# Kernel tuning notes

Hardware: AMD Instinct MI355X
Metric: run time of the kernel (lower is better)

## Reference

```python
import jax, jax.numpy as jnp
import numpy as np


def setup_inputs() -> dict:
    key = jax.random.key(0)
    L, N, Q, C = 6, 64, 64, 256
    hs_pair = jax.random.normal(key, (L, N, Q, C), dtype=jnp.float32)
    return {"hs_pair": hs_pair}


def _merge_step(centers):
    # centers: [L, N, Q, C] -> [L, N, Q-1, C]
    L, N, Q, C = centers.shape
    # pairwise Euclidean distance via gram matrix (avoids [L,N,Q,Q,C] diff tensor)
    sq = jnp.sum(centers * centers, axis=-1)                      # [L,N,Q]
    gram = jnp.einsum('lnqc,lnpc->lnqp', centers, centers)        # [L,N,Q,Q]
    d2 = sq[..., :, None] + sq[..., None, :] - 2.0 * gram
    dist = jnp.sqrt(jnp.maximum(d2, 0.0))                         # [L,N,Q,Q]
    dist = dist + jnp.max(dist) * jnp.eye(Q, dtype=dist.dtype)
    idx = jnp.argmin(dist.reshape(L, N, Q * Q), axis=2)           # [L,N]
    x, y = idx // Q, idx % Q                                      # row-major argmin => x < y
    cx = jnp.take_along_axis(centers, x[:, :, None, None], axis=2)[:, :, 0]  # [L,N,C]
    cy = jnp.take_along_axis(centers, y[:, :, None, None], axis=2)[:, :, 0]  # [L,N,C]
    merged = (cx + cy) * 0.5
    last = centers[:, :, -1]                                      # [L,N,C]
    qr = jnp.arange(Q)
    mask_x = (qr[None, None, :] == x[:, :, None])[..., None]      # [L,N,Q,1]
    mask_y = (qr[None, None, :] == y[:, :, None])[..., None]
    centers = jnp.where(mask_x, merged[:, :, None, :], centers)
    centers = jnp.where(mask_y, last[:, :, None, :], centers)
    return centers[:, :, :-1]


def reference(hs_pair):
    centers = hs_pair
    Q0 = centers.shape[2]
    # Q-2 sequential merges; each iteration has a distinct static shape,
    # so a Python loop (unrolled under jit) is the correct structure.
    for _ in range(Q0 - 2):
        centers = _merge_step(centers)
    return centers  # [L, N, 2, C]
```

## Files before the change

### kernel.cpp

```cpp
#include <hip/hip_runtime.h>
#include <stdint.h>

#define NSLICE 384
#define QMAX   64
#define CDIM   256
#define NTHR   512

#define SW(r,c) ((r)*QMAX + ((c)^(r)))

__device__ __forceinline__ float dpp_sum64(float v) {
#define DPP_ADD(c) v += __int_as_float(__builtin_amdgcn_update_dpp(0, __float_as_int(v), c, 0xf, 0xf, true))
    DPP_ADD(0x111);
    DPP_ADD(0x112);
    DPP_ADD(0x114);
    DPP_ADD(0x118);
    DPP_ADD(0x142);
    DPP_ADD(0x143);
#undef DPP_ADD
    return v;
}

template<int CTRL>
__device__ __forceinline__ unsigned dpp_min_step(unsigned v) {
    unsigned o = (unsigned)__builtin_amdgcn_update_dpp((int)v, (int)v, CTRL, 0xf, 0xf, false);
    return v < o ? v : o;
}

__device__ __forceinline__ unsigned wave_min_bcast(unsigned v) {
    v = dpp_min_step<0x111>(v);
    v = dpp_min_step<0x112>(v);
    v = dpp_min_step<0x114>(v);
    v = dpp_min_step<0x118>(v);
    v = dpp_min_step<0x142>(v);
    v = dpp_min_step<0x143>(v);
    return (unsigned)__builtin_amdgcn_readlane((int)v, 63);
}

__device__ __forceinline__ unsigned oct_min_all(unsigned v) {
    v = dpp_min_step<0xB1>(v);
    v = dpp_min_step<0x4E>(v);
    v = dpp_min_step<0x124>(v);
    return v;
}

__launch_bounds__(NTHR, 4)
__global__ void hca_kernel(const float* __restrict__ in, float* __restrict__ out) {
    __shared__ __align__(16) float cen[QMAX * CDIM];
    __shared__ __align__(16) float dist[QMAX * QMAX];
    unsigned long long* const scratch = (unsigned long long*)(dist + 63 * QMAX);

    const int tid  = threadIdx.x;
    const int lane = tid & 63;
    const int w    = tid >> 6;
    const int slice = blockIdx.x;
    const float* src = in + (size_t)slice * (QMAX * CDIM);
    float* dst = out + (size_t)slice * (2 * CDIM);

    {
        const float4* s4 = (const float4*)src;
        float4* c4 = (float4*)cen;
        #pragma unroll
        for (int i = 0; i < (QMAX * CDIM / 4) / NTHR; ++i)
            c4[tid + i * NTHR] = s4[tid + i * NTHR];
    }
    __syncthreads();

    {
        float4 A[8];
        #pragma unroll
        for (int r = 0; r < 8; ++r)
            A[r] = ((const float4*)(cen + (w + 8 * r) * CDIM))[lane];

        #pragma unroll
        for (int r = 0; r < 8; ++r) {
            float t = A[r].x * A[r].x;
            t = fmaf(A[r].y, A[r].y, t); t = fmaf(A[r].z, A[r].z, t); t = fmaf(A[r].w, A[r].w, t);
            float s = dpp_sum64(t);
            if (lane == 63) dist[(w + 8 * r) * QMAX] = s;
        }
        __syncthreads();

        float sqq[8];
        #pragma unroll
        for (int r = 0; r < 8; ++r) sqq[r] = dist[(w + 8 * r) * QMAX];
        for (int p = 1; p < QMAX; ++p) {
            const float4 b = ((const float4*)(cen + p * CDIM))[lane];
            const float sqp = dist[p * QMAX];
            #pragma unroll
            for (int r = 0; r < 8; ++r) {
                const int q = w + 8 * r;
                if (q < p) {
                    float t = A[r].x * b.x;
                    t = fmaf(A[r].y, b.y, t); t = fmaf(A[r].z, b.z, t); t = fmaf(A[r].w, b.w, t);
                    float s = dpp_sum64(t);
                    if (lane == 63) {
                        float d2 = sqq[r] + sqp - 2.0f * s;
                        float d  = sqrtf(fmaxf(d2, 0.0f));
                        dist[SW(q, p)] = d;
                        dist[SW(p, q)] = d;
                    }
                }
            }
        }
    }
    __syncthreads();

    unsigned flat0, d0bits;
    {
        unsigned bdb = 0xFFFFFFFFu, bidx = 0xFFFu;
        for (int i = 0; i < 16; ++i) {
            float4 dv = ((const float4*)dist)[i * 64 + lane];
            const int rr  = 4 * i + (lane >> 4);
            const int cc0 = (lane & 15) * 4;
            #pragma unroll
            for (int e = 0; e < 4; ++e) {
                int cc = cc0 + e;
                int c  = cc ^ rr;
                unsigned db = __float_as_uint((&dv.x)[e]);
                unsigned idx = (unsigned)(rr * 64 + c);
                bool ok = (cc != 0);
                bool lt = ok & ((db < bdb) | ((db == bdb) & (idx < bidx)));
                bdb  = lt ? db : bdb;
                bidx = lt ? idx : bidx;
            }
        }
        d0bits = wave_min_bcast(bdb);
        unsigned cand = (bdb == d0bits) ? bidx : 0xFFFFFFFFu;
        flat0 = wave_min_bcast(cand);
    }
    __syncthreads();

    for (int Q = QMAX; Q > 2; --Q) {
        int x, y; unsigned dxyb;
        if (Q == QMAX) {
            x = (int)(flat0 >> 6); y = (int)(flat0 & 63); dxyb = d0bits;
        } else {
            unsigned long long k = scratch[lane & 7];
            unsigned hi = (unsigned)(k >> 32), lo = (unsigned)k;
            unsigned ghi = oct_min_all(hi);
            unsigned c2  = (hi == ghi) ? lo : 0xFFFFFFFFu;
            unsigned flat = oct_min_all(c2);
            x = (int)(flat >> 6); y = (int)(flat & 63);
            dxyb = ghi;
        }

        if (w == 0) {
            const int p = lane;
            const bool act = (p < Q - 1) && (p != x);
            const int p_old = (p == y) ? (Q - 1) : p;
            float dxp = 0.0f, dyp = 0.0f;
            if (act) {
                dxp = dist[SW(x, p_old)];
                dyp = dist[SW(y, p_old)];
            }
            const bool mv = (y != Q - 1) && (lane < Q - 1) && (lane != x) && (lane != y);
            float rowQ1 = 0.0f, colQ1 = 0.0f;
            if (mv) {
                rowQ1 = dist[SW(Q - 1, lane)];
                colQ1 = dist[SW(lane, Q - 1)];
            }
            const float dxy = __uint_as_float(dxyb);
            float t = 0.5f * (dxp * dxp + dyp * dyp) - 0.25f * (dxy * dxy);
            float d = sqrtf(fmaxf(t, 0.0f));
            if (mv) {
                dist[SW(y, lane)] = rowQ1;
                dist[SW(lane, y)] = colQ1;
            }
            if (act) {
                dist[SW(x, p)] = d;
                dist[SW(p, x)] = d;
            }
        }
        if (w == 1) {
            const float4 cx = ((const float4*)(cen + x * CDIM))[lane];
            const float4 cy = ((const float4*)(cen + y * CDIM))[lane];
            const float4 cq = ((const float4*)(cen + (Q - 1) * CDIM))[lane];
            float4 m;
            m.x = (cx.x + cy.x) * 0.5f; m.y = (cx.y + cy.y) * 0.5f;
            m.z = (cx.z + cy.z) * 0.5f; m.w = (cx.w + cy.w) * 0.5f;
            ((float4*)(cen + x * CDIM))[lane] = m;
            if (y != Q - 1)
                ((float4*)(cen + y * CDIM))[lane] = cq;
        }
        __syncthreads();

        if (Q > 3) {
            const int Qs = Q - 1;
            unsigned bdb = 0xFFFFFFFFu, bidx = 0xFFFu;
            #pragma unroll
            for (int ii = 0; ii < 2; ++ii) {
                const int i = 2 * w + ii;
                if (4 * i < Qs) {
                    float4 dv = ((const float4*)dist)[i * 64 + lane];
                    const int rr  = 4 * i + (lane >> 4);
                    const int cc0 = (lane & 15) * 4;
                    #pragma unroll
                    for (int e = 0; e < 4; ++e) {
                        int cc = cc0 + e;
                        int c  = cc ^ rr;
                        unsigned db = __float_as_uint((&dv.x)[e]);
                        unsigned idx = (unsigned)(rr * 64 + c);
                        bool ok = (rr < Qs) & (c < Qs) & (cc != 0);
                        bool lt = ok & ((db < bdb) | ((db == bdb) & (idx < bidx)));
                        bdb  = lt ? db : bdb;
                        bidx = lt ? idx : bidx;
                    }
                }
            }
            unsigned gd   = wave_min_bcast(bdb);
            unsigned cand = (bdb == gd) ? bidx : 0xFFFFFFFFu;
            unsigned gidx = wave_min_bcast(cand);
            if (lane == 0) scratch[w] = ((unsigned long long)gd << 32) | gidx;
        }
        __syncthreads();
    }

    for (int i = tid; i < 2 * CDIM; i += NTHR)
        dst[i] = cen[i];
}

extern "C" void kernel_launch(void* const* d_in, const int* in_sizes, int n_in,
                              void* d_out, int out_size, void* d_ws, size_t ws_size,
                              hipStream_t stream) {
    (void)in_sizes; (void)n_in; (void)d_ws; (void)ws_size; (void)out_size;
    const float* in = (const float*)d_in[0];
    float* out = (float*)d_out;
    hca_kernel<<<NSLICE, NTHR, 0, stream>>>(in, out);
}
```

Baseline: 136.0 us.

## Maintain per-row nearest-neighbor cache instead of full distance rescans each merge

Replaces the per-iteration full scan of the upper-triangular distance matrix with a per-row (min distance, column) cache held in double-buffered shared arrays placed in the freed last centroid row. Only rows whose cached nearest column was x or y, plus row x, are rescanned, spread across waves. The other rows are updated incrementally by comparing against the new distance to x. The global argmin then reduces the per-row keys with a wave-wide min. This cuts the O(Q^2) scan per step to roughly O(Q) work, at the cost of more complex bookkeeping and tie-ordering that must match the reference argmin exactly.

```diff
diff --git a/kernel.cpp b/kernel.cpp
--- a/kernel.cpp
+++ b/kernel.cpp
@@ -36,18 +36,14 @@
     return (unsigned)__builtin_amdgcn_readlane((int)v, 63);
 }
 
-__device__ __forceinline__ unsigned oct_min_all(unsigned v) {
-    v = dpp_min_step<0xB1>(v);
-    v = dpp_min_step<0x4E>(v);
-    v = dpp_min_step<0x124>(v);
-    return v;
-}
-
 __launch_bounds__(NTHR, 4)
 __global__ void hca_kernel(const float* __restrict__ in, float* __restrict__ out) {
     __shared__ __align__(16) float cen[QMAX * CDIM];
     __shared__ __align__(16) float dist[QMAX * QMAX];
-    unsigned long long* const scratch = (unsigned long long*)(dist + 63 * QMAX);
+    unsigned* const khi0 = (unsigned*)(cen + 63 * CDIM);
+    unsigned* const klo0 = khi0 + QMAX;
+    unsigned* const khi1 = khi0 + 2 * QMAX;
+    unsigned* const klo1 = khi0 + 3 * QMAX;
 
     const int tid  = threadIdx.x;
     const int lane = tid & 63;
@@ -135,13 +131,15 @@
         if (Q == QMAX) {
             x = (int)(flat0 >> 6); y = (int)(flat0 & 63); dxyb = d0bits;
         } else {
-            unsigned long long k = scratch[lane & 7];
-            unsigned hi = (unsigned)(k >> 32), lo = (unsigned)k;
-            unsigned ghi = oct_min_all(hi);
-            unsigned c2  = (hi == ghi) ? lo : 0xFFFFFFFFu;
-            unsigned flat = oct_min_all(c2);
-            x = (int)(flat >> 6); y = (int)(flat & 63);
-            dxyb = ghi;
+            const unsigned pr = (unsigned)((Q + 1) & 1);
+            const unsigned* khi_s = pr ? khi1 : khi0;
+            const unsigned* klo_s = pr ? klo1 : klo0;
+            unsigned hi = (lane < Q) ? khi_s[lane] : 0xFFFFFFFFu;
+            unsigned gd = wave_min_bcast(hi);
+            unsigned lo = ((lane < Q) & (hi == gd)) ? klo_s[lane] : 0xFFFFFFFFu;
+            unsigned flat = wave_min_bcast(lo);
+            x = (int)((flat >> 6) & 63); y = (int)(flat & 63);
+            dxyb = gd;
         }
 
         if (w == 0) {
@@ -185,32 +183,48 @@
         __syncthreads();
 
         if (Q > 3) {
-            const int Qs = Q - 1;
-            unsigned bdb = 0xFFFFFFFFu, bidx = 0xFFFu;
-            #pragma unroll
-            for (int ii = 0; ii < 2; ++ii) {
-                const int i = 2 * w + ii;
-                if (4 * i < Qs) {
-                    float4 dv = ((const float4*)dist)[i * 64 + lane];
-                    const int rr  = 4 * i + (lane >> 4);
-                    const int cc0 = (lane & 15) * 4;
-                    #pragma unroll
-                    for (int e = 0; e < 4; ++e) {
-                        int cc = cc0 + e;
-                        int c  = cc ^ rr;
-                        unsigned db = __float_as_uint((&dv.x)[e]);
-                        unsigned idx = (unsigned)(rr * 64 + c);
-                        bool ok = (rr < Qs) & (c < Qs) & (cc != 0);
-                        bool lt = ok & ((db < bdb) | ((db == bdb) & (idx < bidx)));
-                        bdb  = lt ? db : bdb;
-                        bidx = lt ? idx : bidx;
-                    }
+            const int Qn = Q - 1;
+            const unsigned pw = (unsigned)(Q & 1);
+            unsigned* const khi_d = pw ? khi1 : khi0;
+            unsigned* const klo_d = pw ? klo1 : klo0;
+
+            auto rescan = [&](int rr) {
+                unsigned dd = 0xFFFFFFFFu;
+                if (lane < Qn && lane != rr) dd = __float_as_uint(dist[SW(rr, lane)]);
+                unsigned gdv = wave_min_bcast(dd);
+                unsigned cc = (dd == gdv) ? (unsigned)lane : 0xFFFFFFFFu;
+                unsigned gc = wave_min_bcast(cc);
+                if (lane == 0) { khi_d[rr] = gdv; klo_d[rr] = (unsigned)((rr << 6) | (int)gc); }
+            };
+
+            if (Q == QMAX) {
+                for (int rr = w; rr < Qn; rr += 8) rescan(rr);
+            } else {
+                const unsigned* khi_s = pw ? khi0 : khi1;
+                const unsigned* klo_s = pw ? klo0 : klo1;
+                const int r = lane;
+                const bool live = (r < Qn) && (r != x);
+                const int srcw = (r == y) ? (Q - 1) : r;
+                unsigned oldlo = live ? klo_s[srcw] : 0xFFFFFFFFu;
+                unsigned oldcol = oldlo & 63u;
+                bool resc = live && ((oldcol == (unsigned)x) || (oldcol == (unsigned)y));
+                unsigned long long mask = __ballot(resc) | (1ull << x);
+                if (w == 0 && live && !resc) {
+                    unsigned oldhi = khi_s[srcw];
+                    unsigned col = (oldcol == (unsigned)(Q - 1)) ? (unsigned)y : oldcol;
+                    unsigned dxb = __float_as_uint(dist[SW(r, x)]);
+                    bool takex = (dxb < oldhi) || ((dxb == oldhi) && ((unsigned)x < col));
+                    khi_d[r] = takex ? dxb : oldhi;
+                    klo_d[r] = (unsigned)((r << 6) | (int)(takex ? (unsigned)x : col));
                 }
-            }
-            unsigned gd   = wave_min_bcast(bdb);
-            unsigned cand = (bdb == gd) ? bidx : 0xFFFFFFFFu;
-            unsigned gidx = wave_min_bcast(cand);
-            if (lane == 0) scratch[w] = ((unsigned long long)gd << 32) | gidx;
+                int i = 0; unsigned long long mm = mask;
+                while (mm) {
+                    int rr = __builtin_ctzll(mm);
+                    mm &= mm - 1;
+                    if ((i & 7) == w) rescan(rr);
+                    ++i;
+                }
+            }
         }
         __syncthreads();
     }
```

Result: slower. 318.1 us (+133.9%).

## Split argmin into min-then-index passes and mask dead rows with infinity

Applied to the files above, without the earlier changes.

The per-step argmin scan becomes two passes: a branch-free min over raw distance bits, then a second pass that finds the smallest flat index equal to that minimum. Bounds and diagonal checks are removed by writing +inf into the retired row and column of the distance matrix on each step, and by masking the scratch row in the last chunk. The first-step scan is unrolled with all 16 float4 chunks held in registers. This cuts compare and select work in the serial 62-step loop, at the cost of extra LDS writes and higher register pressure.

```diff
diff --git a/kernel.cpp b/kernel.cpp
--- a/kernel.cpp
+++ b/kernel.cpp
@@ -7,6 +7,7 @@
 #define NTHR   512
 
 #define SW(r,c) ((r)*QMAX + ((c)^(r)))
+#define INF_F  __int_as_float(0x7F800000)
 
 __device__ __forceinline__ float dpp_sum64(float v) {
 #define DPP_ADD(c) v += __int_as_float(__builtin_amdgcn_update_dpp(0, __float_as_int(v), c, 0xf, 0xf, true))
@@ -105,28 +106,40 @@
     }
     __syncthreads();
 
+    auto chunk_min = [&](const float4& dv, unsigned& part) {
+        unsigned u0 = __float_as_uint(dv.x), u1 = __float_as_uint(dv.y);
+        unsigned u2 = __float_as_uint(dv.z), u3 = __float_as_uint(dv.w);
+        unsigned m01 = u0 < u1 ? u0 : u1;
+        unsigned m23 = u2 < u3 ? u2 : u3;
+        unsigned m = m01 < m23 ? m01 : m23;
+        part = part < m ? part : m;
+    };
+    auto chunk_idx = [&](int i, const float4& dv, unsigned g, unsigned& bi) {
+        const int rr  = 4 * i + (lane >> 4);
+        const int rb  = rr * 64;
+        const int cc0 = (lane & 15) * 4;
+        #pragma unroll
+        for (int e = 0; e < 4; ++e) {
+            unsigned db  = __float_as_uint((&dv.x)[e]);
+            unsigned idx = (unsigned)(rb + ((cc0 + e) ^ rr));
+            if (db == g) bi = idx < bi ? idx : bi;
+        }
+    };
+
     unsigned flat0, d0bits;
     {
-        unsigned bdb = 0xFFFFFFFFu, bidx = 0xFFFu;
+        unsigned part = 0xFFFFFFFFu;
+        float4 dv[16];
+        #pragma unroll
         for (int i = 0; i < 16; ++i) {
-            float4 dv = ((const float4*)dist)[i * 64 + lane];
-            const int rr  = 4 * i + (lane >> 4);
-            const int cc0 = (lane & 15) * 4;
-            #pragma unroll
-            for (int e = 0; e < 4; ++e) {
-                int cc = cc0 + e;
-                int c  = cc ^ rr;
-                unsigned db = __float_as_uint((&dv.x)[e]);
-                unsigned idx = (unsigned)(rr * 64 + c);
-                bool ok = (cc != 0);
-                bool lt = ok & ((db < bdb) | ((db == bdb) & (idx < bidx)));
-                bdb  = lt ? db : bdb;
-                bidx = lt ? idx : bidx;
-            }
-        }
-        d0bits = wave_min_bcast(bdb);
-        unsigned cand = (bdb == d0bits) ? bidx : 0xFFFFFFFFu;
-        flat0 = wave_min_bcast(cand);
+            dv[i] = ((const float4*)dist)[i * 64 + lane];
+            chunk_min(dv[i], part);
+        }
+        d0bits = wave_min_bcast(part);
+        unsigned bi = 0xFFFFFFFFu;
+        #pragma unroll
+        for (int i = 0; i < 16; ++i) chunk_idx(i, dv[i], d0bits, bi);
+        flat0 = wave_min_bcast(bi);
     }
     __syncthreads();
 
@@ -140,7 +153,7 @@
             unsigned ghi = oct_min_all(hi);
             unsigned c2  = (hi == ghi) ? lo : 0xFFFFFFFFu;
             unsigned flat = oct_min_all(c2);
-            x = (int)(flat >> 6); y = (int)(flat & 63);
+            x = (int)((flat >> 6) & 63); y = (int)(flat & 63);
             dxyb = ghi;
         }
 
@@ -153,18 +166,22 @@
                 dxp = dist[SW(x, p_old)];
                 dyp = dist[SW(y, p_old)];
             }
-            const bool mv = (y != Q - 1) && (lane < Q - 1) && (lane != x) && (lane != y);
+            const bool mv = (y != Q - 1) && (p < Q - 1) && (p != x) && (p != y);
             float rowQ1 = 0.0f, colQ1 = 0.0f;
             if (mv) {
-                rowQ1 = dist[SW(Q - 1, lane)];
-                colQ1 = dist[SW(lane, Q - 1)];
+                rowQ1 = dist[SW(Q - 1, p)];
+                colQ1 = dist[SW(p, Q - 1)];
             }
             const float dxy = __uint_as_float(dxyb);
             float t = 0.5f * (dxp * dxp + dyp * dyp) - 0.25f * (dxy * dxy);
             float d = sqrtf(fmaxf(t, 0.0f));
             if (mv) {
-                dist[SW(y, lane)] = rowQ1;
-                dist[SW(lane, y)] = colQ1;
+                dist[SW(y, p)] = rowQ1;
+                dist[SW(p, y)] = colQ1;
+            }
+            if (p < Q) {
+                dist[SW(Q - 1, p)] = INF_F;
+                dist[SW(p, Q - 1)] = INF_F;
             }
             if (act) {
                 dist[SW(x, p)] = d;
@@ -186,31 +203,27 @@
 
         if (Q > 3) {
             const int Qs = Q - 1;
-            unsigned bdb = 0xFFFFFFFFu, bidx = 0xFFFu;
-            #pragma unroll
-            for (int ii = 0; ii < 2; ++ii) {
-                const int i = 2 * w + ii;
-                if (4 * i < Qs) {
-                    float4 dv = ((const float4*)dist)[i * 64 + lane];
-                    const int rr  = 4 * i + (lane >> 4);
-                    const int cc0 = (lane & 15) * 4;
-                    #pragma unroll
-                    for (int e = 0; e < 4; ++e) {
-                        int cc = cc0 + e;
-                        int c  = cc ^ rr;
-                        unsigned db = __float_as_uint((&dv.x)[e]);
-                        unsigned idx = (unsigned)(rr * 64 + c);
-                        bool ok = (rr < Qs) & (c < Qs) & (cc != 0);
-                        bool lt = ok & ((db < bdb) | ((db == bdb) & (idx < bidx)));
-                        bdb  = lt ? db : bdb;
-                        bidx = lt ? idx : bidx;
-                    }
+            unsigned part = 0xFFFFFFFFu;
+            float4 dv0, dv1;
+            const bool live0 = (4 * w < Qs);
+            const bool live1 = (4 * (w + 8) < Qs);
+            if (live0) {
+                dv0 = ((const float4*)dist)[w * 64 + lane];
+                chunk_min(dv0, part);
+            }
+            if (live1) {
+                dv1 = ((const float4*)dist)[(w + 8) * 64 + lane];
+                if (w + 8 == 15 && lane >= 48) {
+                    dv1.x = INF_F; dv1.y = INF_F; dv1.z = INF_F; dv1.w = INF_F;
                 }
-            }
-            unsigned gd   = wave_min_bcast(bdb);
-            unsigned cand = (bdb == gd) ? bidx : 0xFFFFFFFFu;
-            unsigned gidx = wave_min_bcast(cand);
-            if (lane == 0) scratch[w] = ((unsigned long long)gd << 32) | gidx;
+                chunk_min(dv1, part);
+            }
+            unsigned g = wave_min_bcast(part);
+            unsigned bi = 0xFFFFFFFFu;
+            if (live0) chunk_idx(w, dv0, g, bi);
+            if (live1) chunk_idx(w + 8, dv1, g, bi);
+            unsigned bidx = wave_min_bcast(bi);
+            if (lane == 0) scratch[w] = ((unsigned long long)g << 32) | bidx;
         }
         __syncthreads();
     }
```

New measurement: 129.2 us. 5.0% less time.

## Run merge loop on a single wave with packed 64-bit argmin and no barriers

Applied to the files above, without the earlier changes.

After the distance matrix is built, seven of the eight waves exit and wave 0 runs all merge iterations alone. The per-iteration `__syncthreads` barriers and the shared-memory scratch exchange between waves go away. The argmin now packs the distance bits and the index into one 64-bit key and reduces it with DPP. Rows and columns that have been removed are overwritten with +inf, so the scan needs no bounds masks. The cost is that one wave now scans the whole active region serially each step, giving up the 8-way split of the scan.

```diff
diff --git a/kernel.cpp b/kernel.cpp
--- a/kernel.cpp
+++ b/kernel.cpp
@@ -7,6 +7,7 @@
 #define NTHR   512
 
 #define SW(r,c) ((r)*QMAX + ((c)^(r)))
+#define INF_F  __int_as_float(0x7F800000)
 
 __device__ __forceinline__ float dpp_sum64(float v) {
 #define DPP_ADD(c) v += __int_as_float(__builtin_amdgcn_update_dpp(0, __float_as_int(v), c, 0xf, 0xf, true))
@@ -21,33 +22,30 @@
 }
 
 template<int CTRL>
-__device__ __forceinline__ unsigned dpp_min_step(unsigned v) {
-    unsigned o = (unsigned)__builtin_amdgcn_update_dpp((int)v, (int)v, CTRL, 0xf, 0xf, false);
-    return v < o ? v : o;
+__device__ __forceinline__ unsigned long long dpp_min64_step(unsigned long long v) {
+    unsigned lo = (unsigned)v, hi = (unsigned)(v >> 32);
+    unsigned olo = (unsigned)__builtin_amdgcn_update_dpp((int)lo, (int)lo, CTRL, 0xf, 0xf, false);
+    unsigned ohi = (unsigned)__builtin_amdgcn_update_dpp((int)hi, (int)hi, CTRL, 0xf, 0xf, false);
+    unsigned long long o = ((unsigned long long)ohi << 32) | olo;
+    return o < v ? o : v;
 }
 
-__device__ __forceinline__ unsigned wave_min_bcast(unsigned v) {
-    v = dpp_min_step<0x111>(v);
-    v = dpp_min_step<0x112>(v);
-    v = dpp_min_step<0x114>(v);
-    v = dpp_min_step<0x118>(v);
-    v = dpp_min_step<0x142>(v);
-    v = dpp_min_step<0x143>(v);
-    return (unsigned)__builtin_amdgcn_readlane((int)v, 63);
-}
-
-__device__ __forceinline__ unsigned oct_min_all(unsigned v) {
-    v = dpp_min_step<0xB1>(v);
-    v = dpp_min_step<0x4E>(v);
-    v = dpp_min_step<0x124>(v);
-    return v;
+__device__ __forceinline__ unsigned long long wave_min64_bcast(unsigned long long v) {
+    v = dpp_min64_step<0x111>(v);
+    v = dpp_min64_step<0x112>(v);
+    v = dpp_min64_step<0x114>(v);
+    v = dpp_min64_step<0x118>(v);
+    v = dpp_min64_step<0x142>(v);
+    v = dpp_min64_step<0x143>(v);
+    unsigned lo = (unsigned)__builtin_amdgcn_readlane((int)(unsigned)v, 63);
+    unsigned hi = (unsigned)__builtin_amdgcn_readlane((int)(unsigned)(v >> 32), 63);
+    return ((unsigned long long)hi << 32) | lo;
 }
 
 __launch_bounds__(NTHR, 4)
 __global__ void hca_kernel(const float* __restrict__ in, float* __restrict__ out) {
     __shared__ __align__(16) float cen[QMAX * CDIM];
     __shared__ __align__(16) float dist[QMAX * QMAX];
-    unsigned long long* const scratch = (unsigned long long*)(dist + 63 * QMAX);
 
     const int tid  = threadIdx.x;
     const int lane = tid & 63;
@@ -105,118 +103,68 @@
     }
     __syncthreads();
 
-    unsigned flat0, d0bits;
-    {
-        unsigned bdb = 0xFFFFFFFFu, bidx = 0xFFFu;
-        for (int i = 0; i < 16; ++i) {
-            float4 dv = ((const float4*)dist)[i * 64 + lane];
-            const int rr  = 4 * i + (lane >> 4);
-            const int cc0 = (lane & 15) * 4;
-            #pragma unroll
-            for (int e = 0; e < 4; ++e) {
-                int cc = cc0 + e;
-                int c  = cc ^ rr;
-                unsigned db = __float_as_uint((&dv.x)[e]);
-                unsigned idx = (unsigned)(rr * 64 + c);
-                bool ok = (cc != 0);
-                bool lt = ok & ((db < bdb) | ((db == bdb) & (idx < bidx)));
-                bdb  = lt ? db : bdb;
-                bidx = lt ? idx : bidx;
-            }
+    if (w != 0) return;
+
+    auto scan_chunk = [&](int i, unsigned long long& kmin) {
+        const float4 dv = ((const float4*)dist)[i * 64 + lane];
+        const int rr  = 4 * i + (lane >> 4);
+        const int rb  = rr * 64;
+        const int cc0 = (lane & 15) * 4;
+        #pragma unroll
+        for (int e = 0; e < 4; ++e) {
+            unsigned long long kk =
+                ((unsigned long long)__float_as_uint((&dv.x)[e]) << 32)
+                | (unsigned)(rb + ((cc0 + e) ^ rr));
+            kmin = kk < kmin ? kk : kmin;
         }
-        d0bits = wave_min_bcast(bdb);
-        unsigned cand = (bdb == d0bits) ? bidx : 0xFFFFFFFFu;
-        flat0 = wave_min_bcast(cand);
-    }
-    __syncthreads();
+    };
+
+    unsigned long long kmin = ~0ull;
+    #pragma unroll
+    for (int i = 0; i < 16; ++i) scan_chunk(i, kmin);
+    kmin = wave_min64_bcast(kmin);
 
     for (int Q = QMAX; Q > 2; --Q) {
-        int x, y; unsigned dxyb;
-        if (Q == QMAX) {
-            x = (int)(flat0 >> 6); y = (int)(flat0 & 63); dxyb = d0bits;
-        } else {
-            unsigned long long k = scratch[lane & 7];
-            unsigned hi = (unsigned)(k >> 32), lo = (unsigned)k;
-            unsigned ghi = oct_min_all(hi);
-            unsigned c2  = (hi == ghi) ? lo : 0xFFFFFFFFu;
-            unsigned flat = oct_min_all(c2);
-            x = (int)(flat >> 6); y = (int)(flat & 63);
-            dxyb = ghi;
-        }
+        const int Qm1 = Q - 1;
+        const unsigned fl = (unsigned)kmin & 0xFFFu;
+        const int x = (int)(fl >> 6), y = (int)(fl & 63);
+        const float dxy = __uint_as_float((unsigned)(kmin >> 32));
 
-        if (w == 0) {
-            const int p = lane;
-            const bool act = (p < Q - 1) && (p != x);
-            const int p_old = (p == y) ? (Q - 1) : p;
-            float dxp = 0.0f, dyp = 0.0f;
-            if (act) {
-                dxp = dist[SW(x, p_old)];
-                dyp = dist[SW(y, p_old)];
-            }
-            const bool mv = (y != Q - 1) && (lane < Q - 1) && (lane != x) && (lane != y);
-            float rowQ1 = 0.0f, colQ1 = 0.0f;
-            if (mv) {
-                rowQ1 = dist[SW(Q - 1, lane)];
-                colQ1 = dist[SW(lane, Q - 1)];
-            }
-            const float dxy = __uint_as_float(dxyb);
-            float t = 0.5f * (dxp * dxp + dyp * dyp) - 0.25f * (dxy * dxy);
-            float d = sqrtf(fmaxf(t, 0.0f));
-            if (mv) {
-                dist[SW(y, lane)] = rowQ1;
-                dist[SW(lane, y)] = colQ1;
-            }
-            if (act) {
-                dist[SW(x, p)] = d;
-                dist[SW(p, x)] = d;
-            }
-        }
-        if (w == 1) {
-            const float4 cx = ((const float4*)(cen + x * CDIM))[lane];
-            const float4 cy = ((const float4*)(cen + y * CDIM))[lane];
-            const float4 cq = ((const float4*)(cen + (Q - 1) * CDIM))[lane];
-            float4 m;
-            m.x = (cx.x + cy.x) * 0.5f; m.y = (cx.y + cy.y) * 0.5f;
-            m.z = (cx.z + cy.z) * 0.5f; m.w = (cx.w + cy.w) * 0.5f;
-            ((float4*)(cen + x * CDIM))[lane] = m;
-            if (y != Q - 1)
-                ((float4*)(cen + y * CDIM))[lane] = cq;
-        }
-        __syncthreads();
+        const float4 cx  = ((const float4*)(cen + x * CDIM))[lane];
+        const float4 cy4 = ((const float4*)(cen + y * CDIM))[lane];
+        const float4 cq  = ((const float4*)(cen + Qm1 * CDIM))[lane];
+
+        const int p = lane;
+        const bool act = (p < Qm1) && (p != x);
+        const int p_old = (p == y) ? Qm1 : p;
+        float dxp = 0.0f, dyp = 0.0f;
+        if (act) { dxp = dist[SW(x, p_old)]; dyp = dist[SW(y, p_old)]; }
+        const bool mv = (y != Qm1) && (p < Qm1) && (p != x) && (p != y);
+        float rowQ1 = 0.0f, colQ1 = 0.0f;
+        if (mv) { rowQ1 = dist[SW(Qm1, p)]; colQ1 = dist[SW(p, Qm1)]; }
+        float t = 0.5f * (dxp * dxp + dyp * dyp) - 0.25f * (dxy * dxy);
+        float d = sqrtf(fmaxf(t, 0.0f));
+        if (mv) { dist[SW(y, p)] = rowQ1; dist[SW(p, y)] = colQ1; }
+        if (p < Q) { dist[SW(Qm1, p)] = INF_F; dist[SW(p, Qm1)] = INF_F; }
+        if (act) { dist[SW(x, p)] = d; dist[SW(p, x)] = d; }
+
+        float4 m;
+        m.x = (cx.x + cy4.x) * 0.5f; m.y = (cx.y + cy4.y) * 0.5f;
+        m.z = (cx.z + cy4.z) * 0.5f; m.w = (cx.w + cy4.w) * 0.5f;
+        ((float4*)(cen + x * CDIM))[lane] = m;
+        if (y != Qm1) ((float4*)(cen + y * CDIM))[lane] = cq;
 
         if (Q > 3) {
-            const int Qs = Q - 1;
-            unsigned bdb = 0xFFFFFFFFu, bidx = 0xFFFu;
-            #pragma unroll
-            for (int ii = 0; ii < 2; ++ii) {
-                const int i = 2 * w + ii;
-                if (4 * i < Qs) {
-                    float4 dv = ((const float4*)dist)[i * 64 + lane];
-                    const int rr  = 4 * i + (lane >> 4);
-                    const int cc0 = (lane & 15) * 4;
-                    #pragma unroll
-                    for (int e = 0; e < 4; ++e) {
-                        int cc = cc0 + e;
-                        int c  = cc ^ rr;
-                        unsigned db = __float_as_uint((&dv.x)[e]);
-                        unsigned idx = (unsigned)(rr * 64 + c);
-                        bool ok = (rr < Qs) & (c < Qs) & (cc != 0);
-                        bool lt = ok & ((db < bdb) | ((db == bdb) & (idx < bidx)));
-                        bdb  = lt ? db : bdb;
-                        bidx = lt ? idx : bidx;
-                    }
-                }
-            }
-            unsigned gd   = wave_min_bcast(bdb);
-            unsigned cand = (bdb == gd) ? bidx : 0xFFFFFFFFu;
-            unsigned gidx = wave_min_bcast(cand);
-            if (lane == 0) scratch[w] = ((unsigned long long)gd << 32) | gidx;
+            const int nc = ((Q - 2) >> 2) + 1;
+            kmin = ~0ull;
+            for (int i = 0; i < nc; ++i) scan_chunk(i, kmin);
+            kmin = wave_min64_bcast(kmin);
         }
-        __syncthreads();
     }
 
-    for (int i = tid; i < 2 * CDIM; i += NTHR)
-        dst[i] = cen[i];
+    #pragma unroll
+    for (int i = 0; i < 2; ++i)
+        ((float4*)dst)[lane + 64 * i] = ((const float4*)cen)[lane + 64 * i];
 }
 
 extern "C" void kernel_launch(void* const* d_in, const int* in_sizes, int n_in,
```

Result: slower. 147.2 us (+8.2%).
